# Kernel tuning notes

Measured on AMD Instinct MI355X. Metric: run time of the kernel, lower is better.

Reference implementation:

```python
import jax, jax.numpy as jnp
import numpy as np

B, D_IN, H, D_OUT = 4096, 4096, 2048, 1000
LN_EPS = 1e-5


def setup_inputs() -> dict:
    key = jax.random.key(0)
    ks = jax.random.split(key, 8)
    s_in = 1.0 / np.sqrt(H)  # torch RNN init: U(-1/sqrt(H), 1/sqrt(H))
    inp = {
        "x": jax.random.normal(ks[0], (B, D_IN), dtype=jnp.float32),
        "W_ih0": jax.random.uniform(ks[1], (H, D_IN), jnp.float32, -s_in, s_in),
        "b_ih0": jax.random.uniform(ks[2], (H,), jnp.float32, -s_in, s_in),
        "b_hh0": jax.random.uniform(ks[3], (H,), jnp.float32, -s_in, s_in),
        "W_ih1": jax.random.uniform(ks[4], (H, H), jnp.float32, -s_in, s_in),
        "b_ih1": jax.random.uniform(ks[5], (H,), jnp.float32, -s_in, s_in),
        "b_hh1": jax.random.uniform(ks[6], (H,), jnp.float32, -s_in, s_in),
        "ln_g": jnp.ones((2 * H,), jnp.float32),
        "ln_b": jnp.zeros((2 * H,), jnp.float32),
        "fc_W": jax.random.uniform(ks[7], (D_OUT, 2 * H), jnp.float32, -1.0 / np.sqrt(2 * H), 1.0 / np.sqrt(2 * H)),
        "fc_b": jnp.zeros((D_OUT,), jnp.float32),
    }
    return inp


def reference(x, W_ih0, b_ih0, b_hh0, W_ih1, b_ih1, b_hh1, ln_g, ln_b, fc_W, fc_b):
    # seq_len == 1, h0 == 0 -> W_hh terms vanish; only biases remain.
    h1 = jnp.tanh(x @ W_ih0.T + b_ih0 + b_hh0)          # [B, H]
    h2 = jnp.tanh(h1 @ W_ih1.T + b_ih1 + b_hh1)         # [B, H]
    # last_hidden == mean_pooled (single step) -> concat duplicates h2
    combined = jnp.concatenate([h2, h2], axis=1)        # [B, 2H]
    mu = combined.mean(axis=-1, keepdims=True)
    var = combined.var(axis=-1, keepdims=True)
    normed = (combined - mu) * jax.lax.rsqrt(var + LN_EPS) * ln_g + ln_b
    # dropout is identity in eval mode
    return normed @ fc_W.T + fc_b                        # [B, D_OUT]
```

## Files before the change

### kernel.cpp

```cpp
#include <hip/hip_runtime.h>
#include <hip/hip_bf16.h>

typedef __attribute__((ext_vector_type(8))) unsigned short ushort8;
typedef __attribute__((ext_vector_type(8))) __bf16 bf16x8;
typedef __attribute__((ext_vector_type(4))) float f32x4;
typedef __attribute__((ext_vector_type(4))) float floatx4;

__device__ __forceinline__ unsigned short f2bf(float f) {
    unsigned u = __builtin_bit_cast(unsigned, f);
    u += 0x7fffu + ((u >> 16) & 1u);
    return (unsigned short)(u >> 16);
}
__device__ __forceinline__ float bf2f(unsigned short h) {
    unsigned u = ((unsigned)h) << 16;
    return __builtin_bit_cast(float, u);
}

__device__ __forceinline__ void gload_lds16(const void* g, void* l) {
    __builtin_amdgcn_global_load_lds(
        (const __attribute__((address_space(1))) void*)g,
        (__attribute__((address_space(3))) void*)l,
        16, 0, 0);
}

#define BAR()   asm volatile("s_barrier" ::: "memory")
#define VMW(n)  asm volatile("s_waitcnt vmcnt(" #n ")" ::: "memory")

__global__ __launch_bounds__(256) void cvt_f2bf(const float* __restrict__ in,
                                                unsigned short* __restrict__ out,
                                                int n8) {
    int i = blockIdx.x * 256 + threadIdx.x;
    if (i >= n8) return;
    floatx4 a = ((const floatx4*)in)[2 * i];
    floatx4 b = ((const floatx4*)in)[2 * i + 1];
    ushort8 o;
#pragma unroll
    for (int j = 0; j < 4; ++j) { o[j] = f2bf(a[j]); o[4 + j] = f2bf(b[j]); }
    ((ushort8*)out)[i] = o;
}

__global__ __launch_bounds__(256) void weff_kernel(const float* __restrict__ fcW,
                                                   const float* __restrict__ lng,
                                                   const float* __restrict__ lnb,
                                                   const float* __restrict__ fcb,
                                                   unsigned short* __restrict__ weff,
                                                   float* __restrict__ cc,
                                                   float* __restrict__ wsum) {
    int o = blockIdx.x;
    int tid = threadIdx.x;
    if (o >= 1000) {
        ushort8 z = {0, 0, 0, 0, 0, 0, 0, 0};
        ((ushort8*)(weff + (size_t)o * 2048))[tid] = z;
        if (tid == 0) { cc[o] = 0.f; wsum[o] = 0.f; }
        return;
    }
    const float* wrow = fcW + (size_t)o * 4096;
    int j0 = tid * 8;
    floatx4 wa  = *(const floatx4*)(wrow + j0);
    floatx4 wb  = *(const floatx4*)(wrow + j0 + 4);
    floatx4 wa2 = *(const floatx4*)(wrow + 2048 + j0);
    floatx4 wb2 = *(const floatx4*)(wrow + 2048 + j0 + 4);
    floatx4 ga  = *(const floatx4*)(lng + j0);
    floatx4 gb  = *(const floatx4*)(lng + j0 + 4);
    floatx4 ga2 = *(const floatx4*)(lng + 2048 + j0);
    floatx4 gb2 = *(const floatx4*)(lng + 2048 + j0 + 4);
    floatx4 ba  = *(const floatx4*)(lnb + j0);
    floatx4 bb  = *(const floatx4*)(lnb + j0 + 4);
    floatx4 ba2 = *(const floatx4*)(lnb + 2048 + j0);
    floatx4 bb2 = *(const floatx4*)(lnb + 2048 + j0 + 4);
    ushort8 o8;
    float acc = 0.f, ws = 0.f;
#pragma unroll
    for (int j = 0; j < 4; ++j) {
        o8[j] = f2bf(ga[j] * wa[j] + ga2[j] * wa2[j]);
        acc += ba[j] * wa[j] + ba2[j] * wa2[j];
        ws  += bf2f(o8[j]);
        o8[4 + j] = f2bf(gb[j] * wb[j] + gb2[j] * wb2[j]);
        acc += bb[j] * wb[j] + bb2[j] * wb2[j];
        ws  += bf2f(o8[4 + j]);
    }
    ((ushort8*)(weff + (size_t)o * 2048))[tid] = o8;
#pragma unroll
    for (int d = 32; d; d >>= 1) { acc += __shfl_down(acc, d); ws += __shfl_down(ws, d); }
    __shared__ float red[4], redw[4];
    if ((tid & 63) == 0) { red[tid >> 6] = acc; redw[tid >> 6] = ws; }
    __syncthreads();
    if (tid == 0) {
        cc[o] = fcb[o] + red[0] + red[1] + red[2] + red[3];
        wsum[o] = redw[0] + redw[1] + redw[2] + redw[3];
    }
}

__global__ __launch_bounds__(256) void ln_stats(const unsigned short* __restrict__ h2,
                                                float2* __restrict__ mur) {
    int row = blockIdx.x, tid = threadIdx.x;
    ushort8 v = ((const ushort8*)(h2 + (size_t)row * 2048))[tid];
    float s = 0.f, s2 = 0.f;
#pragma unroll
    for (int j = 0; j < 8; ++j) { float f = bf2f(v[j]); s += f; s2 += f * f; }
#pragma unroll
    for (int d = 32; d; d >>= 1) { s += __shfl_down(s, d); s2 += __shfl_down(s2, d); }
    __shared__ float rs_[4], rs2_[4];
    if ((tid & 63) == 0) { rs_[tid >> 6] = s; rs2_[tid >> 6] = s2; }
    __syncthreads();
    if (tid == 0) {
        float S = rs_[0] + rs_[1] + rs_[2] + rs_[3];
        float S2 = rs2_[0] + rs2_[1] + rs2_[2] + rs2_[3];
        float mu = S * (1.f / 2048.f);
        float var = S2 * (1.f / 2048.f) - mu * mu;
        mur[row] = make_float2(mu, rsqrtf(var + 1e-5f));
    }
}

template <int EPI, int NJ>
__global__ __launch_bounds__(512, 2) void gemm_rp(const unsigned short* __restrict__ A,
                                                  const unsigned short* __restrict__ B,
                                                  int M, int N, int K,
                                                  const float* __restrict__ bias0,
                                                  const float* __restrict__ bias1,
                                                  void* __restrict__ Cout, int ncols,
                                                  const float2* __restrict__ mur,
                                                  const float* __restrict__ wsum) {
    extern __shared__ char smem[];
    constexpr int BUFSZ = 16384 + NJ * 8192;
    const int tid = threadIdx.x;
    const int lane = tid & 63, wid = tid >> 6;
    const int wm = wid >> 2, wn = wid & 3;
    const int fr = lane & 15, g = lane >> 4;

    const int nwg = gridDim.x * gridDim.y;
    const int fid = blockIdx.y * gridDim.x + blockIdx.x;
    const int cpx = nwg >> 3;
    const int sw = (fid & 7) * cpx + (fid >> 3);
    const int bx = sw % gridDim.x, by = sw / gridDim.x;
    const int row0 = by * 128, col0 = bx * (64 * NJ);

    const int tg = tid >> 3;
    const int tcE = ((tid & 7) ^ (tg & 7)) * 8;

    auto stage = [&](int kt, char* buf) {
#pragma unroll
        for (int r = 0; r < 2; ++r)
            gload_lds16(A + (size_t)(row0 + r * 64 + tg) * K + kt * 64 + tcE,
                        buf + r * 8192 + wid * 1024);
#pragma unroll
        for (int rr = 0; rr < NJ; ++rr)
            gload_lds16(B + (size_t)(col0 + rr * 64 + tg) * K + kt * 64 + tcE,
                        buf + 16384 + rr * 8192 + wid * 1024);
    };

    const int xorv = (fr & 7) << 4;
    auto readFrags = [&](bf16x8 (&fa)[4][2], bf16x8 (&fb)[NJ][2], const char* buf) {
#pragma unroll
        for (int m = 0; m < 4; ++m)
#pragma unroll
            for (int kh = 0; kh < 2; ++kh)
                fa[m][kh] = __builtin_bit_cast(bf16x8, *(const ushort8*)(
                    buf + (wm * 64 + m * 16 + fr) * 128 + ((kh * 64 + g * 16) ^ xorv)));
#pragma unroll
        for (int n = 0; n < NJ; ++n)
#pragma unroll
            for (int kh = 0; kh < 2; ++kh)
                fb[n][kh] = __builtin_bit_cast(bf16x8, *(const ushort8*)(
                    buf + 16384 + (wn * (16 * NJ) + n * 16 + fr) * 128 + ((kh * 64 + g * 16) ^ xorv)));
    };

    f32x4 acc[4][NJ];
#pragma unroll
    for (int i = 0; i < 4; ++i)
#pragma unroll
        for (int j = 0; j < NJ; ++j) acc[i][j] = f32x4{0.f, 0.f, 0.f, 0.f};

    auto domfma = [&](bf16x8 (&fa)[4][2], bf16x8 (&fb)[NJ][2]) {
        __builtin_amdgcn_s_setprio(1);
#pragma unroll
        for (int m = 0; m < 4; ++m)
#pragma unroll
            for (int n = 0; n < NJ; ++n)
#pragma unroll
                for (int kh = 0; kh < 2; ++kh)
                    acc[m][n] = __builtin_amdgcn_mfma_f32_16x16x32_bf16(fa[m][kh], fb[n][kh], acc[m][n], 0, 0, 0);
        __builtin_amdgcn_s_setprio(0);
    };

    bf16x8 aX[4][2], bX[NJ][2], aY[4][2], bY[NJ][2];

    stage(0, smem); stage(1, smem + BUFSZ);
    if constexpr (NJ == 4) VMW(6); else VMW(4);
    BAR();
    readFrags(aX, bX, smem);

    const int NT = K >> 6;
    for (int t = 0; t < NT; t += 2) {
        if (t + 2 < NT) {
            stage(t + 2, smem + ((t + 2) % 3) * BUFSZ);
            if constexpr (NJ == 4) VMW(6); else VMW(4);
        } else {
            VMW(0);
        }
        BAR();
        readFrags(aY, bY, smem + ((t + 1) % 3) * BUFSZ);
        domfma(aX, bX);

        if (t + 2 < NT) {
            if (t + 3 < NT) {
                stage(t + 3, smem + ((t + 3) % 3) * BUFSZ);
                if constexpr (NJ == 4) VMW(6); else VMW(4);
            } else {
                VMW(0);
            }
            BAR();
            readFrags(aX, bX, smem + ((t + 2) % 3) * BUFSZ);
        }
        domfma(aY, bY);
    }

#pragma unroll
    for (int i = 0; i < 4; ++i) {
        int rbase = row0 + wm * 64 + i * 16 + g * 4;
        if (EPI == 0) {
#pragma unroll
            for (int j = 0; j < NJ; ++j) {
                int col = col0 + wn * (16 * NJ) + j * 16 + fr;
                float bsum = bias0[col] + bias1[col];
                unsigned short* O = (unsigned short*)Cout;
#pragma unroll
                for (int r = 0; r < 4; ++r)
                    O[(size_t)(rbase + r) * N + col] = f2bf(tanhf(acc[i][j][r] + bsum));
            }
        } else {
            float2 mr[4];
#pragma unroll
            for (int r = 0; r < 4; ++r) mr[r] = mur[rbase + r];
#pragma unroll
            for (int j = 0; j < NJ; ++j) {
                int col = col0 + wn * (16 * NJ) + j * 16 + fr;
                if (col < ncols) {
                    float ws = wsum[col];
                    float ccv = bias0[col];
                    float* O = (float*)Cout;
#pragma unroll
                    for (int r = 0; r < 4; ++r)
                        O[(size_t)(rbase + r) * ncols + col] =
                            mr[r].y * (acc[i][j][r] - mr[r].x * ws) + ccv;
                }
            }
        }
    }
}

extern "C" void kernel_launch(void* const* d_in, const int* in_sizes, int n_in,
                              void* d_out, int out_size, void* d_ws, size_t ws_size,
                              hipStream_t stream) {
    const float* x   = (const float*)d_in[0];
    const float* W0  = (const float*)d_in[1];
    const float* bi0 = (const float*)d_in[2];
    const float* bh0 = (const float*)d_in[3];
    const float* W1  = (const float*)d_in[4];
    const float* bi1 = (const float*)d_in[5];
    const float* bh1 = (const float*)d_in[6];
    const float* lng = (const float*)d_in[7];
    const float* lnb = (const float*)d_in[8];
    const float* fcW = (const float*)d_in[9];
    const float* fcb = (const float*)d_in[10];
    float* out = (float*)d_out;

    char* w = (char*)d_ws;
    unsigned short* xb   = (unsigned short*)(w);
    unsigned short* w0b  = (unsigned short*)(w + 33554432ull);
    unsigned short* w1b  = (unsigned short*)(w + 50331648ull);
    unsigned short* h1   = (unsigned short*)(w + 58720256ull);
    unsigned short* h2   = (unsigned short*)(w + 75497472ull);
    unsigned short* weff = (unsigned short*)(w + 92274688ull);
    float* cc            = (float*)(w + 96468992ull);
    float* wsum          = (float*)(w + 96473088ull);
    float2* mur          = (float2*)(w + 96477184ull);

    const int SHM0 = 3 * (16384 + 4 * 8192);
    const int SHM1 = 3 * (16384 + 2 * 8192);
    (void)hipFuncSetAttribute((const void*)gemm_rp<0, 4>,
                              hipFuncAttributeMaxDynamicSharedMemorySize, SHM0);
    (void)hipFuncSetAttribute((const void*)gemm_rp<1, 2>,
                              hipFuncAttributeMaxDynamicSharedMemorySize, SHM1);

    cvt_f2bf<<<8192, 256, 0, stream>>>(x,  xb,  2097152);
    cvt_f2bf<<<4096, 256, 0, stream>>>(W0, w0b, 1048576);
    cvt_f2bf<<<2048, 256, 0, stream>>>(W1, w1b, 524288);
    weff_kernel<<<1024, 256, 0, stream>>>(fcW, lng, lnb, fcb, weff, cc, wsum);
    gemm_rp<0, 4><<<dim3(8, 32), 512, SHM0, stream>>>(xb, w0b, 4096, 2048, 4096,
                                                      bi0, bh0, h1, 2048, nullptr, nullptr);
    gemm_rp<0, 4><<<dim3(8, 32), 512, SHM0, stream>>>(h1, w1b, 4096, 2048, 2048,
                                                      bi1, bh1, h2, 2048, nullptr, nullptr);
    ln_stats<<<4096, 256, 0, stream>>>(h2, mur);
    gemm_rp<1, 2><<<dim3(8, 32), 512, SHM1, stream>>>(h2, weff, 4096, 1024, 2048,
                                                      cc, nullptr, out, 1000, mur, wsum);
}
```

Before: 174.8 us.

## Use 256x256 split-K GEMM with bf16 partials and separate bias-tanh reduce

Replaces the two hidden-layer GEMMs with a new 256x256-tile kernel that splits K into two halves (grid z=2). Each half writes bf16 partial sums, and a separate reduce_tanh kernel adds them with the biases and applies tanh. The larger tile raises arithmetic intensity and LDS reuse, and split-K keeps 256 workgroups in flight. In exchange it adds extra partial-sum traffic and kernel launches, rounds the partial sums to bf16 (a precision loss), and uses a double-buffered pipeline with more barriers.

```diff
diff --git a/kernel.cpp b/kernel.cpp
--- a/kernel.cpp
+++ b/kernel.cpp
@@ -24,7 +24,9 @@
 }
 
 #define BAR()   asm volatile("s_barrier" ::: "memory")
-#define VMW(n)  asm volatile("s_waitcnt vmcnt(" #n ")" ::: "memory")
+#define VMW4()  asm volatile("s_waitcnt vmcnt(4)" ::: "memory")
+#define VMW2()  asm volatile("s_waitcnt vmcnt(2)" ::: "memory")
+#define VMW0()  asm volatile("s_waitcnt vmcnt(0)" ::: "memory")
 
 __global__ __launch_bounds__(256) void cvt_f2bf(const float* __restrict__ in,
                                                 unsigned short* __restrict__ out,
@@ -112,6 +114,186 @@
     }
 }
 
+__global__ __launch_bounds__(256) void reduce_tanh(const unsigned short* __restrict__ P0,
+                                                   const unsigned short* __restrict__ P1,
+                                                   const float* __restrict__ b0,
+                                                   const float* __restrict__ b1,
+                                                   unsigned short* __restrict__ out) {
+    int i = blockIdx.x * 256 + threadIdx.x;
+    ushort8 p0 = ((const ushort8*)P0)[i];
+    ushort8 p1 = ((const ushort8*)P1)[i];
+    int c0 = (i * 8) & 2047;
+    floatx4 ba = *(const floatx4*)(b0 + c0), bb = *(const floatx4*)(b0 + c0 + 4);
+    floatx4 ca = *(const floatx4*)(b1 + c0), cb = *(const floatx4*)(b1 + c0 + 4);
+    ushort8 o;
+#pragma unroll
+    for (int j = 0; j < 4; ++j) {
+        o[j]     = f2bf(tanhf(bf2f(p0[j])     + bf2f(p1[j])     + ba[j] + ca[j]));
+        o[4 + j] = f2bf(tanhf(bf2f(p0[4 + j]) + bf2f(p1[4 + j]) + bb[j] + cb[j]));
+    }
+    ((ushort8*)out)[i] = o;
+}
+
+__global__ __launch_bounds__(512, 2) void gemm256(const unsigned short* __restrict__ A,
+                                                  const unsigned short* __restrict__ B,
+                                                  int Ks, int KP, int N,
+                                                  unsigned short* __restrict__ Pa,
+                                                  unsigned short* __restrict__ Pb) {
+    extern __shared__ char smem[];
+    const int tid = threadIdx.x;
+    const int lane = tid & 63, wid = tid >> 6;
+    const int wm = wid >> 2, wn = wid & 3;
+    const int fr = lane & 15, g = lane >> 4;
+    const int kp = blockIdx.z;
+
+    const int gx = gridDim.x;
+    const int nwg = gx * gridDim.y;
+    const int fid = blockIdx.y * gx + blockIdx.x;
+    const int cpx = nwg >> 3;
+    const int sw = (fid & 7) * cpx + (fid >> 3);
+    const int bx = sw % gx, by = sw / gx;
+    const int row0 = by * 256, col0 = bx * 256;
+    const int kbase = kp * KP;
+
+    char* bufA0 = smem;
+    char* bufB0 = smem + 32768;
+
+    const int rl = tid >> 3;
+    const int sl = tid & 7;
+    const int scol = ((sl ^ (rl & 7)) * 8);
+
+    auto stageA = [&](int kt, int half, char* bufb) {
+        const size_t koff = (size_t)(kbase + kt * 64 + scol);
+#pragma unroll
+        for (int gg = 0; gg < 2; ++gg) {
+            int r = half * 128 + gg * 64;
+            gload_lds16(A + (size_t)(row0 + r + rl) * Ks + koff,
+                        bufb + r * 128 + wid * 1024);
+        }
+    };
+    auto stageB = [&](int kt, int half, char* bufb) {
+        const size_t koff = (size_t)(kbase + kt * 64 + scol);
+#pragma unroll
+        for (int gg = 0; gg < 2; ++gg) {
+            int r = half * 128 + gg * 64;
+            gload_lds16(B + (size_t)(col0 + r + rl) * Ks + koff,
+                        bufb + 32768 + r * 128 + wid * 1024);
+        }
+    };
+
+    const int xorv = (fr & 7) << 4;
+    auto readA = [&](bf16x8 (&fa)[4][2], const char* bufb, int hi) {
+#pragma unroll
+        for (int m = 0; m < 4; ++m) {
+            int row = hi * 128 + wm * 64 + m * 16 + fr;
+#pragma unroll
+            for (int kh = 0; kh < 2; ++kh)
+                fa[m][kh] = __builtin_bit_cast(bf16x8, *(const ushort8*)(
+                    bufb + row * 128 + ((kh * 64 + g * 16) ^ xorv)));
+        }
+    };
+    auto readB = [&](bf16x8 (&fb)[2][2], const char* bufb, int bh) {
+#pragma unroll
+        for (int n = 0; n < 2; ++n) {
+            int row = bh * 128 + wn * 32 + n * 16 + fr;
+#pragma unroll
+            for (int kh = 0; kh < 2; ++kh)
+                fb[n][kh] = __builtin_bit_cast(bf16x8, *(const ushort8*)(
+                    bufb + 32768 + row * 128 + ((kh * 64 + g * 16) ^ xorv)));
+        }
+    };
+
+    f32x4 acc[8][4];
+#pragma unroll
+    for (int i = 0; i < 8; ++i)
+#pragma unroll
+        for (int j = 0; j < 4; ++j) acc[i][j] = f32x4{0.f, 0.f, 0.f, 0.f};
+
+    bf16x8 aF[4][2], b0[2][2], b1[2][2];
+
+    stageA(0, 0, smem); stageB(0, 0, smem); stageB(0, 1, smem); stageA(0, 1, smem);
+
+    const int NT = KP >> 6;
+    for (int t = 0; t < NT; ++t) {
+        char* rb = smem + (t & 1) * 65536;
+        char* wb = smem + ((t + 1) & 1) * 65536;
+        const bool st = (t + 1) < NT;
+
+        VMW4();
+        BAR();
+        if (st) stageA(t + 1, 0, wb);
+        readA(aF, rb, 0);
+        readB(b0, rb, 0);
+        __builtin_amdgcn_s_setprio(1);
+#pragma unroll
+        for (int m = 0; m < 4; ++m)
+#pragma unroll
+            for (int n = 0; n < 2; ++n)
+#pragma unroll
+                for (int kh = 0; kh < 2; ++kh)
+                    acc[m][n] = __builtin_amdgcn_mfma_f32_16x16x32_bf16(aF[m][kh], b0[n][kh], acc[m][n], 0, 0, 0);
+        __builtin_amdgcn_s_setprio(0);
+        BAR();
+
+        if (st) { VMW4(); } else { VMW2(); }
+        BAR();
+        if (st) stageB(t + 1, 0, wb);
+        readB(b1, rb, 1);
+        __builtin_amdgcn_s_setprio(1);
+#pragma unroll
+        for (int m = 0; m < 4; ++m)
+#pragma unroll
+            for (int n = 0; n < 2; ++n)
+#pragma unroll
+                for (int kh = 0; kh < 2; ++kh)
+                    acc[m][2 + n] = __builtin_amdgcn_mfma_f32_16x16x32_bf16(aF[m][kh], b1[n][kh], acc[m][2 + n], 0, 0, 0);
+        __builtin_amdgcn_s_setprio(0);
+        BAR();
+
+        if (st) { VMW4(); } else { VMW0(); }
+        BAR();
+        if (st) stageB(t + 1, 1, wb);
+        readA(aF, rb, 1);
+        __builtin_amdgcn_s_setprio(1);
+#pragma unroll
+        for (int m = 0; m < 4; ++m)
+#pragma unroll
+            for (int n = 0; n < 2; ++n)
+#pragma unroll
+                for (int kh = 0; kh < 2; ++kh)
+                    acc[4 + m][2 + n] = __builtin_amdgcn_mfma_f32_16x16x32_bf16(aF[m][kh], b1[n][kh], acc[4 + m][2 + n], 0, 0, 0);
+        __builtin_amdgcn_s_setprio(0);
+        BAR();
+
+        if (st) stageA(t + 1, 1, wb);
+        __builtin_amdgcn_s_setprio(1);
+#pragma unroll
+        for (int m = 0; m < 4; ++m)
+#pragma unroll
+            for (int n = 0; n < 2; ++n)
+#pragma unroll
+                for (int kh = 0; kh < 2; ++kh)
+                    acc[4 + m][n] = __builtin_amdgcn_mfma_f32_16x16x32_bf16(aF[m][kh], b0[n][kh], acc[4 + m][n], 0, 0, 0);
+        __builtin_amdgcn_s_setprio(0);
+        BAR();
+    }
+
+    unsigned short* P = kp ? Pb : Pa;
+#pragma unroll
+    for (int i = 0; i < 8; ++i) {
+        int hi = i >> 2, m = i & 3;
+        int rbase = row0 + hi * 128 + wm * 64 + m * 16 + g * 4;
+#pragma unroll
+        for (int j = 0; j < 4; ++j) {
+            int bh = j >> 1, n = j & 1;
+            int col = col0 + bh * 128 + wn * 32 + n * 16 + fr;
+#pragma unroll
+            for (int r = 0; r < 4; ++r)
+                P[(size_t)(rbase + r) * N + col] = f2bf(acc[i][j][r]);
+        }
+    }
+}
+
 template <int EPI, int NJ>
 __global__ __launch_bounds__(512, 2) void gemm_rp(const unsigned short* __restrict__ A,
                                                   const unsigned short* __restrict__ B,
@@ -186,7 +368,8 @@
     bf16x8 aX[4][2], bX[NJ][2], aY[4][2], bY[NJ][2];
 
     stage(0, smem); stage(1, smem + BUFSZ);
-    if constexpr (NJ == 4) VMW(6); else VMW(4);
+    if constexpr (NJ == 4) { asm volatile("s_waitcnt vmcnt(6)" ::: "memory"); }
+    else                   { asm volatile("s_waitcnt vmcnt(4)" ::: "memory"); }
     BAR();
     readFrags(aX, bX, smem);
 
@@ -194,9 +377,10 @@
     for (int t = 0; t < NT; t += 2) {
         if (t + 2 < NT) {
             stage(t + 2, smem + ((t + 2) % 3) * BUFSZ);
-            if constexpr (NJ == 4) VMW(6); else VMW(4);
+            if constexpr (NJ == 4) { asm volatile("s_waitcnt vmcnt(6)" ::: "memory"); }
+            else                   { asm volatile("s_waitcnt vmcnt(4)" ::: "memory"); }
         } else {
-            VMW(0);
+            VMW0();
         }
         BAR();
         readFrags(aY, bY, smem + ((t + 1) % 3) * BUFSZ);
@@ -205,9 +389,10 @@
         if (t + 2 < NT) {
             if (t + 3 < NT) {
                 stage(t + 3, smem + ((t + 3) % 3) * BUFSZ);
-                if constexpr (NJ == 4) VMW(6); else VMW(4);
+                if constexpr (NJ == 4) { asm volatile("s_waitcnt vmcnt(6)" ::: "memory"); }
+                else                   { asm volatile("s_waitcnt vmcnt(4)" ::: "memory"); }
             } else {
-                VMW(0);
+                VMW0();
             }
             BAR();
             readFrags(aX, bX, smem + ((t + 2) % 3) * BUFSZ);
@@ -275,11 +460,15 @@
     float* cc            = (float*)(w + 96468992ull);
     float* wsum          = (float*)(w + 96473088ull);
     float2* mur          = (float2*)(w + 96477184ull);
-
-    const int SHM0 = 3 * (16384 + 4 * 8192);
+    unsigned short* P1a  = h2;
+    unsigned short* P1b  = (unsigned short*)(w + 96509952ull);
+    unsigned short* P2a  = xb;
+    unsigned short* P2b  = (unsigned short*)(w + 16777216ull);
+
+    const int SHM256 = 131072;
     const int SHM1 = 3 * (16384 + 2 * 8192);
-    (void)hipFuncSetAttribute((const void*)gemm_rp<0, 4>,
-                              hipFuncAttributeMaxDynamicSharedMemorySize, SHM0);
+    (void)hipFuncSetAttribute((const void*)gemm256,
+                              hipFuncAttributeMaxDynamicSharedMemorySize, SHM256);
     (void)hipFuncSetAttribute((const void*)gemm_rp<1, 2>,
                               hipFuncAttributeMaxDynamicSharedMemorySize, SHM1);
 
@@ -287,10 +476,13 @@
     cvt_f2bf<<<4096, 256, 0, stream>>>(W0, w0b, 1048576);
     cvt_f2bf<<<2048, 256, 0, stream>>>(W1, w1b, 524288);
     weff_kernel<<<1024, 256, 0, stream>>>(fcW, lng, lnb, fcb, weff, cc, wsum);
-    gemm_rp<0, 4><<<dim3(8, 32), 512, SHM0, stream>>>(xb, w0b, 4096, 2048, 4096,
-                                                      bi0, bh0, h1, 2048, nullptr, nullptr);
-    gemm_rp<0, 4><<<dim3(8, 32), 512, SHM0, stream>>>(h1, w1b, 4096, 2048, 2048,
-                                                      bi1, bh1, h2, 2048, nullptr, nullptr);
+
+    gemm256<<<dim3(8, 16, 2), 512, SHM256, stream>>>(xb, w0b, 4096, 2048, 2048, P1a, P1b);
+    reduce_tanh<<<4096, 256, 0, stream>>>(P1a, P1b, bi0, bh0, h1);
+
+    gemm256<<<dim3(8, 16, 2), 512, SHM256, stream>>>(h1, w1b, 2048, 1024, 2048, P2a, P2b);
+    reduce_tanh<<<4096, 256, 0, stream>>>(P2a, P2b, bi1, bh1, h2);
+
     ln_stats<<<4096, 256, 0, stream>>>(h2, mur);
     gemm_rp<1, 2><<<dim3(8, 32), 512, SHM1, stream>>>(h2, weff, 4096, 1024, 2048,
                                                       cc, nullptr, out, 1000, mur, wsum);
```

After: 183.9 us. 5.2% more time.

## Replace first two GEMMs with 256x256 split-K kernel plus bias-tanh reduce

Applied to the files above, without the earlier changes.

The two hidden-layer GEMMs move to a new kernel with 256x256 tiles, K split in two across blockIdx.z, double-buffered LDS and explicit sched_group_barrier interleaving of LDS reads with MFMAs. Each split writes bf16 partials to workspace, and a separate reduce_tanh kernel sums them, adds the biases and applies tanh. Larger tiles raise operand reuse, and split-K keeps the grid at 256 workgroups. In exchange it adds extra partial-sum memory traffic, two more launches, and bf16 rounding of the partials before the sum.

```diff
diff --git a/kernel.cpp b/kernel.cpp
--- a/kernel.cpp
+++ b/kernel.cpp
@@ -24,7 +24,10 @@
 }
 
 #define BAR()   asm volatile("s_barrier" ::: "memory")
-#define VMW(n)  asm volatile("s_waitcnt vmcnt(" #n ")" ::: "memory")
+#define VMW0()  asm volatile("s_waitcnt vmcnt(0)" ::: "memory")
+#define LGK0()  asm volatile("s_waitcnt lgkmcnt(0)" ::: "memory")
+#define SGB_DS(n)   __builtin_amdgcn_sched_group_barrier(0x100, n, 0)
+#define SGB_MFMA(n) __builtin_amdgcn_sched_group_barrier(0x008, n, 0)
 
 __global__ __launch_bounds__(256) void cvt_f2bf(const float* __restrict__ in,
                                                 unsigned short* __restrict__ out,
@@ -112,6 +115,145 @@
     }
 }
 
+__global__ __launch_bounds__(256) void reduce_tanh(const unsigned short* __restrict__ P0,
+                                                   const unsigned short* __restrict__ P1,
+                                                   const float* __restrict__ b0,
+                                                   const float* __restrict__ b1,
+                                                   unsigned short* __restrict__ out) {
+    int i = blockIdx.x * 256 + threadIdx.x;
+    ushort8 p0 = ((const ushort8*)P0)[i];
+    ushort8 p1 = ((const ushort8*)P1)[i];
+    int c0 = (i * 8) & 2047;
+    floatx4 ba = *(const floatx4*)(b0 + c0), bb = *(const floatx4*)(b0 + c0 + 4);
+    floatx4 ca = *(const floatx4*)(b1 + c0), cb = *(const floatx4*)(b1 + c0 + 4);
+    ushort8 o;
+#pragma unroll
+    for (int j = 0; j < 4; ++j) {
+        o[j]     = f2bf(tanhf(bf2f(p0[j])     + bf2f(p1[j])     + ba[j] + ca[j]));
+        o[4 + j] = f2bf(tanhf(bf2f(p0[4 + j]) + bf2f(p1[4 + j]) + bb[j] + cb[j]));
+    }
+    ((ushort8*)out)[i] = o;
+}
+
+__global__ __launch_bounds__(512, 2) void gemm256i(const unsigned short* __restrict__ A,
+                                                   const unsigned short* __restrict__ B,
+                                                   int Ks, int KP, int N,
+                                                   unsigned short* __restrict__ Pa,
+                                                   unsigned short* __restrict__ Pb) {
+    extern __shared__ char smem[];
+    const int tid = threadIdx.x;
+    const int lane = tid & 63;
+    const int wid = tid >> 6;
+    const int wm = wid >> 2, wn = wid & 3;
+    const int fr = lane & 15, g = lane >> 4;
+    const int kp = blockIdx.z;
+
+    const int gx = gridDim.x;
+    const int nwg = gx * gridDim.y;
+    const int fid = blockIdx.y * gx + blockIdx.x;
+    const int cpx = nwg >> 3;
+    const int sw = (fid & 7) * cpx + (fid >> 3);
+    const int bx = sw % gx, by = sw / gx;
+    const int row0 = by * 256, col0 = bx * 256;
+    const int kbase = kp * KP;
+
+    const int srow = tid >> 2;
+    const int scole = ((tid & 3) ^ ((tid >> 3) & 3)) << 3;
+    auto stage = [&](int kt, char* buf) {
+        const size_t koff = (size_t)(kbase + kt * 32 + scole);
+#pragma unroll
+        for (int r = 0; r < 2; ++r)
+            gload_lds16(A + (size_t)(row0 + r * 128 + srow) * Ks + koff,
+                        buf + r * 8192 + tid * 16);
+#pragma unroll
+        for (int r = 0; r < 2; ++r)
+            gload_lds16(B + (size_t)(col0 + r * 128 + srow) * Ks + koff,
+                        buf + 16384 + r * 8192 + tid * 16);
+    };
+
+    const int kb = (g * 16) ^ (((fr >> 1) & 3) << 4);
+    const char* pA0 = smem + (wm * 128 + fr) * 64 + kb;
+    const char* pB0 = smem + 16384 + (wn * 64 + fr) * 64 + kb;
+    const char* pA1 = pA0 + 32768;
+    const char* pB1 = pB0 + 32768;
+
+#define LDF(p, off) __builtin_bit_cast(bf16x8, *(const ushort8*)((p) + (off)))
+#define MF4(aC, bC, mm) \
+    acc[mm][0] = __builtin_amdgcn_mfma_f32_16x16x32_bf16(aC[mm], bC[0], acc[mm][0], 0, 0, 0); \
+    acc[mm][1] = __builtin_amdgcn_mfma_f32_16x16x32_bf16(aC[mm], bC[1], acc[mm][1], 0, 0, 0); \
+    acc[mm][2] = __builtin_amdgcn_mfma_f32_16x16x32_bf16(aC[mm], bC[2], acc[mm][2], 0, 0, 0); \
+    acc[mm][3] = __builtin_amdgcn_mfma_f32_16x16x32_bf16(aC[mm], bC[3], acc[mm][3], 0, 0, 0);
+#define SGBCHAIN() \
+    SGB_DS(2); SGB_MFMA(4); SGB_DS(2); SGB_MFMA(4); SGB_DS(2); SGB_MFMA(4); \
+    SGB_DS(2); SGB_MFMA(4); SGB_DS(2); SGB_MFMA(4); SGB_DS(2); SGB_MFMA(4); \
+    SGB_MFMA(4); SGB_MFMA(4);
+#define TILE_BODY(aC, bC, aN, bN, pAn, pBn) do { \
+    bN[0] = LDF(pBn, 0);    bN[1] = LDF(pBn, 1024); \
+    MF4(aC, bC, 0); \
+    bN[2] = LDF(pBn, 2048); bN[3] = LDF(pBn, 3072); \
+    MF4(aC, bC, 1); \
+    aN[0] = LDF(pAn, 0);    aN[1] = LDF(pAn, 1024); \
+    MF4(aC, bC, 2); \
+    aN[2] = LDF(pAn, 2048); aN[3] = LDF(pAn, 3072); \
+    MF4(aC, bC, 3); \
+    aN[4] = LDF(pAn, 4096); aN[5] = LDF(pAn, 5120); \
+    MF4(aC, bC, 4); \
+    aN[6] = LDF(pAn, 6144); aN[7] = LDF(pAn, 7168); \
+    MF4(aC, bC, 5); \
+    MF4(aC, bC, 6); \
+    MF4(aC, bC, 7); \
+    SGBCHAIN(); \
+} while (0)
+
+    f32x4 acc[8][4];
+#pragma unroll
+    for (int i = 0; i < 8; ++i)
+#pragma unroll
+        for (int j = 0; j < 4; ++j) acc[i][j] = f32x4{0.f, 0.f, 0.f, 0.f};
+
+    bf16x8 aX[8], bX[4], aY[8], bY[4];
+
+    stage(0, smem);
+    stage(1, smem + 32768);
+    asm volatile("s_waitcnt vmcnt(4)" ::: "memory");
+    BAR();
+#pragma unroll
+    for (int n = 0; n < 4; ++n) bX[n] = LDF(pB0, n * 1024);
+#pragma unroll
+    for (int m = 0; m < 8; ++m) aX[m] = LDF(pA0, m * 1024);
+
+    const int NT = KP >> 5;
+    for (int t = 0; t < NT - 2; t += 2) {
+        LGK0(); VMW0(); BAR();
+        stage(t + 2, smem);
+        TILE_BODY(aX, bX, aY, bY, pA1, pB1);
+        LGK0(); VMW0(); BAR();
+        stage(t + 3, smem + 32768);
+        TILE_BODY(aY, bY, aX, bX, pA0, pB0);
+    }
+    LGK0(); VMW0(); BAR();
+    TILE_BODY(aX, bX, aY, bY, pA1, pB1);
+#pragma unroll
+    for (int m = 0; m < 8; ++m) { MF4(aY, bY, m); }
+
+    unsigned short* P = kp ? Pb : Pa;
+#pragma unroll
+    for (int m = 0; m < 8; ++m) {
+        int rbase = row0 + wm * 128 + m * 16 + g * 4;
+#pragma unroll
+        for (int n = 0; n < 4; ++n) {
+            int col = col0 + wn * 64 + n * 16 + fr;
+#pragma unroll
+            for (int r = 0; r < 4; ++r)
+                P[(size_t)(rbase + r) * N + col] = f2bf(acc[m][n][r]);
+        }
+    }
+#undef TILE_BODY
+#undef SGBCHAIN
+#undef MF4
+#undef LDF
+}
+
 template <int EPI, int NJ>
 __global__ __launch_bounds__(512, 2) void gemm_rp(const unsigned short* __restrict__ A,
                                                   const unsigned short* __restrict__ B,
@@ -186,7 +328,8 @@
     bf16x8 aX[4][2], bX[NJ][2], aY[4][2], bY[NJ][2];
 
     stage(0, smem); stage(1, smem + BUFSZ);
-    if constexpr (NJ == 4) VMW(6); else VMW(4);
+    if constexpr (NJ == 4) { asm volatile("s_waitcnt vmcnt(6)" ::: "memory"); }
+    else                   { asm volatile("s_waitcnt vmcnt(4)" ::: "memory"); }
     BAR();
     readFrags(aX, bX, smem);
 
@@ -194,9 +337,10 @@
     for (int t = 0; t < NT; t += 2) {
         if (t + 2 < NT) {
             stage(t + 2, smem + ((t + 2) % 3) * BUFSZ);
-            if constexpr (NJ == 4) VMW(6); else VMW(4);
+            if constexpr (NJ == 4) { asm volatile("s_waitcnt vmcnt(6)" ::: "memory"); }
+            else                   { asm volatile("s_waitcnt vmcnt(4)" ::: "memory"); }
         } else {
-            VMW(0);
+            VMW0();
         }
         BAR();
         readFrags(aY, bY, smem + ((t + 1) % 3) * BUFSZ);
@@ -205,9 +349,10 @@
         if (t + 2 < NT) {
             if (t + 3 < NT) {
                 stage(t + 3, smem + ((t + 3) % 3) * BUFSZ);
-                if constexpr (NJ == 4) VMW(6); else VMW(4);
+                if constexpr (NJ == 4) { asm volatile("s_waitcnt vmcnt(6)" ::: "memory"); }
+                else                   { asm volatile("s_waitcnt vmcnt(4)" ::: "memory"); }
             } else {
-                VMW(0);
+                VMW0();
             }
             BAR();
             readFrags(aX, bX, smem + ((t + 2) % 3) * BUFSZ);
@@ -275,11 +420,15 @@
     float* cc            = (float*)(w + 96468992ull);
     float* wsum          = (float*)(w + 96473088ull);
     float2* mur          = (float2*)(w + 96477184ull);
-
-    const int SHM0 = 3 * (16384 + 4 * 8192);
+    unsigned short* P1a  = h2;
+    unsigned short* P1b  = (unsigned short*)(w + 96509952ull);
+    unsigned short* P2a  = xb;
+    unsigned short* P2b  = (unsigned short*)(w + 16777216ull);
+
+    const int SHM256 = 65536;
     const int SHM1 = 3 * (16384 + 2 * 8192);
-    (void)hipFuncSetAttribute((const void*)gemm_rp<0, 4>,
-                              hipFuncAttributeMaxDynamicSharedMemorySize, SHM0);
+    (void)hipFuncSetAttribute((const void*)gemm256i,
+                              hipFuncAttributeMaxDynamicSharedMemorySize, SHM256);
     (void)hipFuncSetAttribute((const void*)gemm_rp<1, 2>,
                               hipFuncAttributeMaxDynamicSharedMemorySize, SHM1);
 
@@ -287,10 +436,13 @@
     cvt_f2bf<<<4096, 256, 0, stream>>>(W0, w0b, 1048576);
     cvt_f2bf<<<2048, 256, 0, stream>>>(W1, w1b, 524288);
     weff_kernel<<<1024, 256, 0, stream>>>(fcW, lng, lnb, fcb, weff, cc, wsum);
-    gemm_rp<0, 4><<<dim3(8, 32), 512, SHM0, stream>>>(xb, w0b, 4096, 2048, 4096,
-                                                      bi0, bh0, h1, 2048, nullptr, nullptr);
-    gemm_rp<0, 4><<<dim3(8, 32), 512, SHM0, stream>>>(h1, w1b, 4096, 2048, 2048,
-                                                      bi1, bh1, h2, 2048, nullptr, nullptr);
+
+    gemm256i<<<dim3(8, 16, 2), 512, SHM256, stream>>>(xb, w0b, 4096, 2048, 2048, P1a, P1b);
+    reduce_tanh<<<4096, 256, 0, stream>>>(P1a, P1b, bi0, bh0, h1);
+
+    gemm256i<<<dim3(8, 16, 2), 512, SHM256, stream>>>(h1, w1b, 2048, 1024, 2048, P2a, P2b);
+    reduce_tanh<<<4096, 256, 0, stream>>>(P2a, P2b, bi1, bh1, h2);
+
     ln_stats<<<4096, 256, 0, stream>>>(h2, mur);
     gemm_rp<1, 2><<<dim3(8, 32), 512, SHM1, stream>>>(h2, weff, 4096, 1024, 2048,
                                                       cc, nullptr, out, 1000, mur, wsum);
```

After: 188.6 us. 1.08x slower.
